# Kernel optimization log

Measured on AMD Instinct MI355X. Metric: run time of the kernel, lower is better.

The kernel has to match this reference:

```python
import jax, jax.numpy as jnp
import numpy as np

ROUTINGS = 3
NUM_CAPSULE = 32
DIM_CAPSULE = 64
K_EPSILON = 1e-7  # keras K.epsilon()


def squash(x, axis=-1):
    s = jnp.sum(jnp.square(x), axis=axis, keepdims=True) + K_EPSILON
    scale = jnp.sqrt(s) / (0.5 + s)
    return scale * x


def setup_inputs() -> dict:
    key = jax.random.key(0)
    k1, k2 = jax.random.split(key)
    B, N_in, D_in = 32, 1024, 512
    u = jax.random.normal(k1, (B, N_in, D_in), dtype=jnp.float32)
    # glorot_uniform for capsule_kernel (conv1d width-1 kernel == dense matrix)
    fan_out = NUM_CAPSULE * DIM_CAPSULE
    limit = float(np.sqrt(6.0 / (D_in + fan_out)))
    W = jax.random.uniform(k2, (D_in, fan_out), jnp.float32, -limit, limit)
    return {"u": u, "W": W}


def reference(u, W):
    B, N_in, _ = u.shape
    # K.conv1d with width-1 kernel == matmul, then reshape
    u_hat = (u @ W).reshape(B, N_in, NUM_CAPSULE, DIM_CAPSULE)
    u_hat = jnp.transpose(u_hat, (0, 2, 1, 3))  # [B, N_out, N_in, D]
    b = jnp.zeros(u_hat.shape[:3], u_hat.dtype)  # [B, N_out, N_in]
    vj = None
    for i in range(ROUTINGS):
        Wv = jax.nn.softmax(b, axis=1)  # softmax over output capsules (axis=1)
        vj = jnp.einsum('bon,bond->bod', Wv, u_hat)  # batch_dot(Wv,u_hat,[2,2])
        if i < ROUTINGS - 1:
            # K.l2_normalize(vj) with default axis=None -> global L2 norm
            norm = jnp.sqrt(jnp.maximum(jnp.sum(jnp.square(vj)), 1e-12))
            vjn = vj / norm
            b = jnp.einsum('bod,bond->bon', vjn, u_hat)  # batch_dot(vj,u_hat,[2,3])
    return squash(vj)
```

## Files before the change

### kernel.cpp

```cpp
#include <hip/hip_runtime.h>
#include <hip/hip_bf16.h>


constexpr int B = 32, N = 1024, K = 512, O = 32, D = 64, F = 2048;
constexpr int NT = 32;
constexpr int ST = 72;

typedef __attribute__((ext_vector_type(8))) short bf16x8;
typedef __attribute__((ext_vector_type(4))) float f32x4;

__device__ inline unsigned int pk_hi(float x, float y) {
  union { __hip_bfloat162 h; unsigned int u; } c;
  c.h = __float22bfloat162_rn(float2{x, y});
  return c.u;
}
__device__ inline unsigned short bf16_1(float x) {
  return (unsigned short)(pk_hi(x, 0.f) & 0xffffu);
}
__device__ inline void split2(float x, unsigned short& h, unsigned short& l) {
  h = bf16_1(x);
  l = bf16_1(x - __uint_as_float((unsigned int)h << 16));
}
__device__ inline float bf2f(unsigned short h) {
  return __uint_as_float((unsigned int)h << 16);
}
__device__ inline int swz(int r) { return ((r >> 3) & 7) << 3; }

__device__ inline bf16x8 frag_row(const unsigned short* p, int r, int k0) {
  return *(const bf16x8*)&p[r * ST + (k0 ^ swz(r))];
}
__device__ inline bf16x8 frag_col(const unsigned short* p, int c, int n0) {
  bf16x8 f;
#pragma unroll
  for (int j = 0; j < 8; j++) {
    int n = n0 + j;
    f[j] = (short)p[n * ST + (c ^ swz(n))];
  }
  return f;
}

__global__ __launch_bounds__(256) void k_prep(const float* __restrict__ u,
                                              float* __restrict__ cs_part,
                                              unsigned short* __restrict__ u_bf) {
  __shared__ float4 red[128];
  int b = blockIdx.x, ntile = blockIdx.y, n0 = ntile * 32;
  int tid = threadIdx.x;
  int kq = (tid & 127) * 4, ng = tid >> 7;
  const float* ub = u + ((size_t)b * N + n0 + ng * 16) * K + kq;
  unsigned short* ubf = u_bf + ((size_t)b * N + n0 + ng * 16) * K + kq;
  float4 a = {0.f, 0.f, 0.f, 0.f};
#pragma unroll
  for (int nn = 0; nn < 16; nn++) {
    float4 v = *(const float4*)&ub[(size_t)nn * K];
    a.x += v.x; a.y += v.y; a.z += v.z; a.w += v.w;
    uint2 p;
    p.x = pk_hi(v.x, v.y);
    p.y = pk_hi(v.z, v.w);
    *(uint2*)&ubf[(size_t)nn * K] = p;
  }
  if (ng) red[tid & 127] = a;
  __syncthreads();
  if (!ng) {
    float4 o = red[tid];
    float* cs = cs_part + ((size_t)b * 32 + ntile) * K + kq;
    cs[0] = (a.x + o.x) * (1.f / 32.f);
    cs[1] = (a.y + o.y) * (1.f / 32.f);
    cs[2] = (a.z + o.z) * (1.f / 32.f);
    cs[3] = (a.w + o.w) * (1.f / 32.f);
  }
}

__global__ __launch_bounds__(512) void k_vjt(const unsigned short* __restrict__ Sp,
                                             const float* __restrict__ cs_part,
                                             const float* __restrict__ W,
                                             float* __restrict__ ssq_part, int slot,
                                             unsigned short* __restrict__ t_hi,
                                             unsigned short* __restrict__ t_lo) {
  __shared__ __align__(16) float s_s[K];
  __shared__ float red[7][D];
  __shared__ __align__(16) float vs[D];
  int bo = blockIdx.x, b = bo >> 5, o = bo & 31;
  int d = threadIdx.x & 63, ks = threadIdx.x >> 6;
  {
    int i = threadIdx.x;
    float a = 0.f;
    if (slot == 0) {
      const float* base = cs_part + (size_t)b * 32 * K;
#pragma unroll
      for (int nt = 0; nt < 32; nt++) a += base[(size_t)nt * K + i];
    } else {
      const unsigned short* base = Sp + ((size_t)b * NT * O + o) * K;
#pragma unroll
      for (int nt = 0; nt < NT; nt++) a += bf2f(base[(size_t)nt * O * K + i]);
    }
    s_s[i] = a;
  }
  __syncthreads();
  float acc = 0.f;
  const float* Wc = W + (size_t)o * D + d;
  for (int k = ks * 64; k < ks * 64 + 64; k += 4) {
    acc += s_s[k] * Wc[(size_t)k * F] + s_s[k + 1] * Wc[(size_t)(k + 1) * F] +
           s_s[k + 2] * Wc[(size_t)(k + 2) * F] + s_s[k + 3] * Wc[(size_t)(k + 3) * F];
  }
  if (ks) red[ks - 1][d] = acc;
  __syncthreads();
  if (ks == 0) {
#pragma unroll
    for (int j = 0; j < 7; j++) acc += red[j][d];
    vs[d] = acc;
    float ss = acc * acc;
#pragma unroll
    for (int m = 32; m >= 1; m >>= 1) ss += __shfl_xor(ss, m, 64);
    if (d == 0) ssq_part[slot * 1024 + bo] = ss;
  }
  __syncthreads();
  {
    int wave = threadIdx.x >> 6, lane = threadIdx.x & 63;
    int rr = lane >> 3, dc = lane & 7;
    float4 va = *(const float4*)&vs[dc * 8];
    float4 vb = *(const float4*)&vs[dc * 8 + 4];
#pragma unroll
    for (int i = 0; i < 8; i++) {
      int kk = wave * 64 + i * 8 + rr;
      const float* Wr = W + (size_t)kk * F + o * 64 + dc * 8;
      float4 wa = *(const float4*)Wr;
      float4 wb = *(const float4*)(Wr + 4);
      float p = wa.x * va.x + wa.y * va.y + wa.z * va.z + wa.w * va.w +
                wb.x * vb.x + wb.y * vb.y + wb.z * vb.z + wb.w * vb.w;
      p += __shfl_xor(p, 1, 64);
      p += __shfl_xor(p, 2, 64);
      p += __shfl_xor(p, 4, 64);
      if (dc == 0) {
        unsigned short h, l;
        split2(p, h, l);
        t_hi[(size_t)bo * K + kk] = h;
        t_lo[(size_t)bo * K + kk] = l;
      }
    }
  }
}

__global__ __launch_bounds__(512) void k_out(const unsigned short* __restrict__ Sp,
                                             const float* __restrict__ W,
                                             float* __restrict__ out) {
  __shared__ __align__(16) float s_s[K];
  __shared__ float red[7][D];
  int bo = blockIdx.x, b = bo >> 5, o = bo & 31;
  int d = threadIdx.x & 63, ks = threadIdx.x >> 6;
  {
    const unsigned short* base = Sp + ((size_t)b * NT * O + o) * K;
    int i = threadIdx.x;
    float a = 0.f;
#pragma unroll
    for (int nt = 0; nt < NT; nt++) a += bf2f(base[(size_t)nt * O * K + i]);
    s_s[i] = a;
  }
  __syncthreads();
  float acc = 0.f;
  const float* Wc = W + (size_t)o * D + d;
  for (int k = ks * 64; k < ks * 64 + 64; k += 4) {
    acc += s_s[k] * Wc[(size_t)k * F] + s_s[k + 1] * Wc[(size_t)(k + 1) * F] +
           s_s[k + 2] * Wc[(size_t)(k + 2) * F] + s_s[k + 3] * Wc[(size_t)(k + 3) * F];
  }
  if (ks) red[ks - 1][d] = acc;
  __syncthreads();
  if (ks == 0) {
#pragma unroll
    for (int j = 0; j < 7; j++) acc += red[j][d];
    float ss = acc * acc;
#pragma unroll
    for (int m = 32; m >= 1; m >>= 1) ss += __shfl_xor(ss, m, 64);
    float s = ss + 1e-7f;
    out[(size_t)bo * D + d] = (sqrtf(s) / (0.5f + s)) * acc;
  }
}

__global__ __launch_bounds__(256, 3) void k_route(const unsigned short* __restrict__ t_hi_g,
                                                  const unsigned short* __restrict__ t_lo_g,
                                                  const unsigned short* __restrict__ u_bf,
                                                  const float* __restrict__ ssq_part,
                                                  int slot,
                                                  unsigned short* __restrict__ Sp) {
  __shared__ unsigned short u_res[8][32 * ST];
  __shared__ unsigned short t_hi[32 * ST], t_lo[32 * ST];
  __shared__ float wv[32 * 36];
  __shared__ float psum[8 * 36];
  __shared__ float mbuf[36];
  unsigned short* wvh = t_hi;
  unsigned short* wvl = t_lo;

  const int b = blockIdx.x, n0 = blockIdx.y * 32;
  const int tid = threadIdx.x, lane = tid & 63, wave = tid >> 6;
  const int m = lane & 15, oct = lane >> 4;
  const unsigned short* ubf = u_bf + ((size_t)b * N + n0) * K;
  const unsigned short* thg = t_hi_g + (size_t)b * O * K;
  const unsigned short* tlg = t_lo_g + (size_t)b * O * K;

  const int sr = tid >> 3, sc8 = (tid & 7) * 8;
  const int scs = sc8 ^ swz(sr);

  uint4 rth = *(const uint4*)&thg[(size_t)sr * K + sc8];
  uint4 rtl = *(const uint4*)&tlg[(size_t)sr * K + sc8];
#pragma unroll
  for (int ch = 0; ch < 8; ch++) {
    *(uint4*)&u_res[ch][sr * ST + scs] =
        *(const uint4*)&ubf[(size_t)sr * K + ch * 64 + sc8];
  }

  const int mo = wave & 1, nt = wave >> 1;
  f32x4 accb = {0.f, 0.f, 0.f, 0.f};
  for (int kcb = 0; kcb < 8; kcb++) {
    __syncthreads();
    *(uint4*)&t_hi[sr * ST + scs] = rth;
    *(uint4*)&t_lo[sr * ST + scs] = rtl;
    __syncthreads();
    if (kcb < 7) {
      rth = *(const uint4*)&thg[(size_t)sr * K + kcb * 64 + 64 + sc8];
      rtl = *(const uint4*)&tlg[(size_t)sr * K + kcb * 64 + 64 + sc8];
    }
    const unsigned short* uc = u_res[kcb];
#pragma unroll
    for (int ks = 0; ks < 64; ks += 32) {
      bf16x8 ah = frag_row(t_hi, mo * 16 + m, ks + oct * 8);
      bf16x8 al = frag_row(t_lo, mo * 16 + m, ks + oct * 8);
      bf16x8 bh = frag_row(uc, nt * 16 + m, ks + oct * 8);
      accb = __builtin_amdgcn_mfma_f32_16x16x32_bf16(ah, bh, accb, 0, 0, 0);
      accb = __builtin_amdgcn_mfma_f32_16x16x32_bf16(al, bh, accb, 0, 0, 0);
    }
  }
  __syncthreads();
  {
    const float* sp = ssq_part + slot * 1024;
    float sa = 0.f;
#pragma unroll
    for (int j = 0; j < 4; j++) sa += sp[tid + j * 256];
    psum[tid & 255] = sa;
    __syncthreads();
    if (tid < 64) {
      float s = psum[tid] + psum[tid + 64] + psum[tid + 128] + psum[tid + 192];
#pragma unroll
      for (int mm = 32; mm >= 1; mm >>= 1) s += __shfl_xor(s, mm, 64);
      if (tid == 0) mbuf[0] = rsqrtf(fmaxf(s, 1e-12f));
    }
    __syncthreads();
  }
  const float nrm_inv = mbuf[0];
  __syncthreads();
#pragma unroll
  for (int r = 0; r < 4; r++)
    wv[(mo * 16 + oct * 4 + r) * 36 + nt * 16 + m] = accb[r] * nrm_inv;
  __syncthreads();

  {
    int n = tid & 31, g = tid >> 5;
    float m4 = -1e30f;
#pragma unroll
    for (int j = 0; j < 4; j++) m4 = fmaxf(m4, wv[(g * 4 + j) * 36 + n]);
    psum[g * 36 + n] = m4;
    __syncthreads();
    if (tid < 32) {
      float mx = psum[tid];
#pragma unroll
      for (int gg = 1; gg < 8; gg++) mx = fmaxf(mx, psum[gg * 36 + tid]);
      mbuf[tid] = mx;
    }
    __syncthreads();
    float mx = mbuf[n];
    float s4 = 0.f;
#pragma unroll
    for (int j = 0; j < 4; j++) {
      float e = __expf(wv[(g * 4 + j) * 36 + n] - mx);
      wv[(g * 4 + j) * 36 + n] = e;
      s4 += e;
    }
    psum[g * 36 + n] = s4;
    __syncthreads();
    if (tid < 32) {
      float s = 0.f;
#pragma unroll
      for (int gg = 0; gg < 8; gg++) s += psum[gg * 36 + tid];
      mbuf[tid] = 1.f / s;
    }
    __syncthreads();
    float inv = mbuf[n];
#pragma unroll
    for (int j = 0; j < 4; j++) {
      unsigned short h, l;
      split2(wv[(g * 4 + j) * 36 + n] * inv, h, l);
      wvh[(g * 4 + j) * ST + n] = h;
      wvl[(g * 4 + j) * ST + n] = l;
    }
  }
  __syncthreads();

  const int mo2 = wave & 1, kp = wave >> 1;
  const int o0 = mo2 * 16;
  bf16x8 a_h = *(const bf16x8*)&wvh[(o0 + m) * ST + oct * 8];
  bf16x8 a_l = *(const bf16x8*)&wvl[(o0 + m) * ST + oct * 8];
  unsigned short* Sb = Sp + ((size_t)b * NT + blockIdx.y) * O * K;
  for (int kcb = 0; kcb < 8; kcb++) {
    const unsigned short* uc = u_res[kcb];
#pragma unroll
    for (int kt = kp * 2; kt < kp * 2 + 2; kt++) {
      int c = kt * 16 + m;
      bf16x8 bh = frag_col(uc, c, oct * 8);
      f32x4 acs = {0.f, 0.f, 0.f, 0.f};
      acs = __builtin_amdgcn_mfma_f32_16x16x32_bf16(a_h, bh, acs, 0, 0, 0);
      acs = __builtin_amdgcn_mfma_f32_16x16x32_bf16(a_l, bh, acs, 0, 0, 0);
#pragma unroll
      for (int r = 0; r < 4; r++)
        Sb[(size_t)(o0 + oct * 4 + r) * K + kcb * 64 + c] = bf16_1(acs[r]);
    }
  }
}

extern "C" void kernel_launch(void* const* d_in, const int* in_sizes, int n_in,
                              void* d_out, int out_size, void* d_ws, size_t ws_size,
                              hipStream_t stream) {
  const float* u = (const float*)d_in[0];
  const float* W = (const float*)d_in[1];
  float* out = (float*)d_out;

  char* ws = (char*)d_ws;
  unsigned short* Sp = (unsigned short*)ws;
  unsigned short* u_bf = Sp + (size_t)B * NT * O * K;
  unsigned short* t_hi = u_bf + (size_t)B * N * K;
  unsigned short* t_lo = t_hi + (size_t)B * O * K;
  float* cs_part = (float*)(t_lo + (size_t)B * O * K);
  float* ssq_part = cs_part + (size_t)B * 32 * K;

  k_prep<<<dim3(B, 32), 256, 0, stream>>>(u, cs_part, u_bf);
  k_vjt<<<B * O, 512, 0, stream>>>(Sp, cs_part, W, ssq_part, 0, t_hi, t_lo);
  k_route<<<dim3(B, NT), 256, 0, stream>>>(t_hi, t_lo, u_bf, ssq_part, 0, Sp);
  k_vjt<<<B * O, 512, 0, stream>>>(Sp, cs_part, W, ssq_part, 1, t_hi, t_lo);
  k_route<<<dim3(B, NT), 256, 0, stream>>>(t_hi, t_lo, u_bf, ssq_part, 1, Sp);
  k_out<<<B * O, 512, 0, stream>>>(Sp, W, out);
}
```

Measured before the change: 190.8 us.

## Process two N-tiles per routing block and read t fragments directly from global

k_route now handles two 32-row tiles of u per block, launching half as many blocks, and hoists the global norm reduction out of the per-tile loop. The hi/lo t operands are no longer staged through shared memory; each wave loads its MFMA fragments straight from global, relying on cache hits. A smaller padded buffer holds the softmax weights, and launch bounds drop from 3 to 2 blocks per CU. The aim is to amortise the norm reduction and cut LDS traffic and syncs, at the cost of uncoalesced global reads, serialised tiles and fewer resident waves.

```diff
diff --git a/kernel.cpp b/kernel.cpp
--- a/kernel.cpp
+++ b/kernel.cpp
@@ -5,6 +5,7 @@
 constexpr int B = 32, N = 1024, K = 512, O = 32, D = 64, F = 2048;
 constexpr int NT = 32;
 constexpr int ST = 72;
+constexpr int STW = 40;
 
 typedef __attribute__((ext_vector_type(8))) short bf16x8;
 typedef __attribute__((ext_vector_type(4))) float f32x4;
@@ -175,66 +176,34 @@
   }
 }
 
-__global__ __launch_bounds__(256, 3) void k_route(const unsigned short* __restrict__ t_hi_g,
+__global__ __launch_bounds__(256, 2) void k_route(const unsigned short* __restrict__ t_hi_g,
                                                   const unsigned short* __restrict__ t_lo_g,
                                                   const unsigned short* __restrict__ u_bf,
                                                   const float* __restrict__ ssq_part,
                                                   int slot,
                                                   unsigned short* __restrict__ Sp) {
   __shared__ unsigned short u_res[8][32 * ST];
-  __shared__ unsigned short t_hi[32 * ST], t_lo[32 * ST];
   __shared__ float wv[32 * 36];
   __shared__ float psum[8 * 36];
   __shared__ float mbuf[36];
-  unsigned short* wvh = t_hi;
-  unsigned short* wvl = t_lo;
-
-  const int b = blockIdx.x, n0 = blockIdx.y * 32;
+  __shared__ unsigned short wvh[32 * STW], wvl[32 * STW];
+
+  const int b = blockIdx.x;
   const int tid = threadIdx.x, lane = tid & 63, wave = tid >> 6;
   const int m = lane & 15, oct = lane >> 4;
-  const unsigned short* ubf = u_bf + ((size_t)b * N + n0) * K;
   const unsigned short* thg = t_hi_g + (size_t)b * O * K;
   const unsigned short* tlg = t_lo_g + (size_t)b * O * K;
 
   const int sr = tid >> 3, sc8 = (tid & 7) * 8;
   const int scs = sc8 ^ swz(sr);
 
-  uint4 rth = *(const uint4*)&thg[(size_t)sr * K + sc8];
-  uint4 rtl = *(const uint4*)&tlg[(size_t)sr * K + sc8];
-#pragma unroll
-  for (int ch = 0; ch < 8; ch++) {
-    *(uint4*)&u_res[ch][sr * ST + scs] =
-        *(const uint4*)&ubf[(size_t)sr * K + ch * 64 + sc8];
-  }
-
-  const int mo = wave & 1, nt = wave >> 1;
-  f32x4 accb = {0.f, 0.f, 0.f, 0.f};
-  for (int kcb = 0; kcb < 8; kcb++) {
-    __syncthreads();
-    *(uint4*)&t_hi[sr * ST + scs] = rth;
-    *(uint4*)&t_lo[sr * ST + scs] = rtl;
-    __syncthreads();
-    if (kcb < 7) {
-      rth = *(const uint4*)&thg[(size_t)sr * K + kcb * 64 + 64 + sc8];
-      rtl = *(const uint4*)&tlg[(size_t)sr * K + kcb * 64 + 64 + sc8];
-    }
-    const unsigned short* uc = u_res[kcb];
-#pragma unroll
-    for (int ks = 0; ks < 64; ks += 32) {
-      bf16x8 ah = frag_row(t_hi, mo * 16 + m, ks + oct * 8);
-      bf16x8 al = frag_row(t_lo, mo * 16 + m, ks + oct * 8);
-      bf16x8 bh = frag_row(uc, nt * 16 + m, ks + oct * 8);
-      accb = __builtin_amdgcn_mfma_f32_16x16x32_bf16(ah, bh, accb, 0, 0, 0);
-      accb = __builtin_amdgcn_mfma_f32_16x16x32_bf16(al, bh, accb, 0, 0, 0);
-    }
-  }
-  __syncthreads();
+  float nrm_inv;
   {
     const float* sp = ssq_part + slot * 1024;
     float sa = 0.f;
 #pragma unroll
     for (int j = 0; j < 4; j++) sa += sp[tid + j * 256];
-    psum[tid & 255] = sa;
+    psum[tid] = sa;
     __syncthreads();
     if (tid < 64) {
       float s = psum[tid] + psum[tid + 64] + psum[tid + 128] + psum[tid + 192];
@@ -243,73 +212,101 @@
       if (tid == 0) mbuf[0] = rsqrtf(fmaxf(s, 1e-12f));
     }
     __syncthreads();
-  }
-  const float nrm_inv = mbuf[0];
-  __syncthreads();
-#pragma unroll
-  for (int r = 0; r < 4; r++)
-    wv[(mo * 16 + oct * 4 + r) * 36 + nt * 16 + m] = accb[r] * nrm_inv;
-  __syncthreads();
-
-  {
-    int n = tid & 31, g = tid >> 5;
-    float m4 = -1e30f;
-#pragma unroll
-    for (int j = 0; j < 4; j++) m4 = fmaxf(m4, wv[(g * 4 + j) * 36 + n]);
-    psum[g * 36 + n] = m4;
-    __syncthreads();
-    if (tid < 32) {
-      float mx = psum[tid];
-#pragma unroll
-      for (int gg = 1; gg < 8; gg++) mx = fmaxf(mx, psum[gg * 36 + tid]);
-      mbuf[tid] = mx;
-    }
-    __syncthreads();
-    float mx = mbuf[n];
-    float s4 = 0.f;
-#pragma unroll
-    for (int j = 0; j < 4; j++) {
-      float e = __expf(wv[(g * 4 + j) * 36 + n] - mx);
-      wv[(g * 4 + j) * 36 + n] = e;
-      s4 += e;
-    }
-    psum[g * 36 + n] = s4;
-    __syncthreads();
-    if (tid < 32) {
-      float s = 0.f;
-#pragma unroll
-      for (int gg = 0; gg < 8; gg++) s += psum[gg * 36 + tid];
-      mbuf[tid] = 1.f / s;
-    }
-    __syncthreads();
-    float inv = mbuf[n];
-#pragma unroll
-    for (int j = 0; j < 4; j++) {
-      unsigned short h, l;
-      split2(wv[(g * 4 + j) * 36 + n] * inv, h, l);
-      wvh[(g * 4 + j) * ST + n] = h;
-      wvl[(g * 4 + j) * ST + n] = l;
-    }
-  }
-  __syncthreads();
-
+    nrm_inv = mbuf[0];
+  }
+
+  const int mo = wave & 1, nt = wave >> 1;
   const int mo2 = wave & 1, kp = wave >> 1;
   const int o0 = mo2 * 16;
-  bf16x8 a_h = *(const bf16x8*)&wvh[(o0 + m) * ST + oct * 8];
-  bf16x8 a_l = *(const bf16x8*)&wvl[(o0 + m) * ST + oct * 8];
-  unsigned short* Sb = Sp + ((size_t)b * NT + blockIdx.y) * O * K;
-  for (int kcb = 0; kcb < 8; kcb++) {
-    const unsigned short* uc = u_res[kcb];
-#pragma unroll
-    for (int kt = kp * 2; kt < kp * 2 + 2; kt++) {
-      int c = kt * 16 + m;
-      bf16x8 bh = frag_col(uc, c, oct * 8);
-      f32x4 acs = {0.f, 0.f, 0.f, 0.f};
-      acs = __builtin_amdgcn_mfma_f32_16x16x32_bf16(a_h, bh, acs, 0, 0, 0);
-      acs = __builtin_amdgcn_mfma_f32_16x16x32_bf16(a_l, bh, acs, 0, 0, 0);
-#pragma unroll
-      for (int r = 0; r < 4; r++)
-        Sb[(size_t)(o0 + oct * 4 + r) * K + kcb * 64 + c] = bf16_1(acs[r]);
+
+  for (int ti = 0; ti < 2; ti++) {
+    const int tile = blockIdx.y * 2 + ti;
+    const unsigned short* ubf = u_bf + ((size_t)b * N + tile * 32) * K;
+
+    __syncthreads();
+#pragma unroll
+    for (int ch = 0; ch < 8; ch++) {
+      *(uint4*)&u_res[ch][sr * ST + scs] =
+          *(const uint4*)&ubf[(size_t)sr * K + ch * 64 + sc8];
+    }
+    __syncthreads();
+
+    f32x4 accb = {0.f, 0.f, 0.f, 0.f};
+    for (int kcb = 0; kcb < 8; kcb++) {
+      const unsigned short* uc = u_res[kcb];
+      const size_t tb = (size_t)(mo * 16 + m) * K + kcb * 64;
+#pragma unroll
+      for (int ks = 0; ks < 64; ks += 32) {
+        bf16x8 ah = *(const bf16x8*)&thg[tb + ks + oct * 8];
+        bf16x8 al = *(const bf16x8*)&tlg[tb + ks + oct * 8];
+        bf16x8 bh = frag_row(uc, nt * 16 + m, ks + oct * 8);
+        accb = __builtin_amdgcn_mfma_f32_16x16x32_bf16(ah, bh, accb, 0, 0, 0);
+        accb = __builtin_amdgcn_mfma_f32_16x16x32_bf16(al, bh, accb, 0, 0, 0);
+      }
+    }
+#pragma unroll
+    for (int r = 0; r < 4; r++)
+      wv[(mo * 16 + oct * 4 + r) * 36 + nt * 16 + m] = accb[r] * nrm_inv;
+    __syncthreads();
+
+    {
+      int n = tid & 31, g = tid >> 5;
+      float m4 = -1e30f;
+#pragma unroll
+      for (int j = 0; j < 4; j++) m4 = fmaxf(m4, wv[(g * 4 + j) * 36 + n]);
+      psum[g * 36 + n] = m4;
+      __syncthreads();
+      if (tid < 32) {
+        float mx = psum[tid];
+#pragma unroll
+        for (int gg = 1; gg < 8; gg++) mx = fmaxf(mx, psum[gg * 36 + tid]);
+        mbuf[tid] = mx;
+      }
+      __syncthreads();
+      float mx = mbuf[n];
+      float s4 = 0.f;
+#pragma unroll
+      for (int j = 0; j < 4; j++) {
+        float e = __expf(wv[(g * 4 + j) * 36 + n] - mx);
+        wv[(g * 4 + j) * 36 + n] = e;
+        s4 += e;
+      }
+      psum[g * 36 + n] = s4;
+      __syncthreads();
+      if (tid < 32) {
+        float s = 0.f;
+#pragma unroll
+        for (int gg = 0; gg < 8; gg++) s += psum[gg * 36 + tid];
+        mbuf[tid] = 1.f / s;
+      }
+      __syncthreads();
+      float inv = mbuf[n];
+#pragma unroll
+      for (int j = 0; j < 4; j++) {
+        unsigned short h, l;
+        split2(wv[(g * 4 + j) * 36 + n] * inv, h, l);
+        wvh[(g * 4 + j) * STW + n] = h;
+        wvl[(g * 4 + j) * STW + n] = l;
+      }
+    }
+    __syncthreads();
+
+    bf16x8 a_h = *(const bf16x8*)&wvh[(o0 + m) * STW + oct * 8];
+    bf16x8 a_l = *(const bf16x8*)&wvl[(o0 + m) * STW + oct * 8];
+    unsigned short* Sb = Sp + ((size_t)b * NT + tile) * O * K;
+    for (int kcb = 0; kcb < 8; kcb++) {
+      const unsigned short* uc = u_res[kcb];
+#pragma unroll
+      for (int kt = kp * 2; kt < kp * 2 + 2; kt++) {
+        int c = kt * 16 + m;
+        bf16x8 bh = frag_col(uc, c, oct * 8);
+        f32x4 acs = {0.f, 0.f, 0.f, 0.f};
+        acs = __builtin_amdgcn_mfma_f32_16x16x32_bf16(a_h, bh, acs, 0, 0, 0);
+        acs = __builtin_amdgcn_mfma_f32_16x16x32_bf16(a_l, bh, acs, 0, 0, 0);
+#pragma unroll
+        for (int r = 0; r < 4; r++)
+          Sb[(size_t)(o0 + oct * 4 + r) * K + kcb * 64 + c] = bf16_1(acs[r]);
+      }
     }
   }
 }
@@ -331,8 +328,8 @@
 
   k_prep<<<dim3(B, 32), 256, 0, stream>>>(u, cs_part, u_bf);
   k_vjt<<<B * O, 512, 0, stream>>>(Sp, cs_part, W, ssq_part, 0, t_hi, t_lo);
-  k_route<<<dim3(B, NT), 256, 0, stream>>>(t_hi, t_lo, u_bf, ssq_part, 0, Sp);
+  k_route<<<dim3(B, NT / 2), 256, 0, stream>>>(t_hi, t_lo, u_bf, ssq_part, 0, Sp);
   k_vjt<<<B * O, 512, 0, stream>>>(Sp, cs_part, W, ssq_part, 1, t_hi, t_lo);
-  k_route<<<dim3(B, NT), 256, 0, stream>>>(t_hi, t_lo, u_bf, ssq_part, 1, Sp);
+  k_route<<<dim3(B, NT / 2), 256, 0, stream>>>(t_hi, t_lo, u_bf, ssq_part, 1, Sp);
   k_out<<<B * O, 512, 0, stream>>>(Sp, W, out);
 }
```

Result: no change. 189.1 us (-0.9%).
